# Performance work log

Measured on AMD Instinct MI355X. Metric: run time of the kernel, lower is better.

The kernel has to match this reference:

```python
import jax, jax.numpy as jnp
import numpy as np

D_MODEL, D_K, D_V, H = 1024, 64, 64, 16
B, NQ, NK = 4, 1024, 1024


def setup_inputs() -> dict:
    key = jax.random.key(0)
    ks = jax.random.split(key, 16)
    xav = lambda k, shape: jax.random.uniform(k, shape, jnp.float32, -1.0, 1.0) * np.sqrt(6.0 / (shape[0] + shape[1])).astype(np.float32)
    return {
        "queries": jax.random.normal(ks[0], (B, NQ, D_MODEL), jnp.float32),
        "keys": jax.random.normal(ks[1], (B, NK, D_MODEL), jnp.float32),
        "values": jax.random.normal(ks[2], (B, NK, D_MODEL), jnp.float32),
        "attention_weights": jax.random.uniform(ks[3], (B, H, NQ, NK), jnp.float32),
        "attention_mask": jax.random.randint(ks[4], (B, H, NQ, NK), 0, 2, jnp.int32),
        "Wq": xav(ks[5], (H * D_K, D_MODEL)), "bq": jnp.zeros((H * D_K,), jnp.float32),
        "Wk": xav(ks[6], (H * D_K, D_MODEL)), "bk": jnp.zeros((H * D_K,), jnp.float32),
        "Wv": xav(ks[7], (H * D_V, D_MODEL)), "bv": jnp.zeros((H * D_V,), jnp.float32),
        "Wo": xav(ks[8], (D_MODEL, H * D_V)), "bo": jnp.zeros((D_MODEL,), jnp.float32),
    }


def reference(queries, keys, values, attention_weights, attention_mask,
              Wq, bq, Wk, bk, Wv, bv, Wo, bo):
    b, nq, _ = queries.shape
    nk = keys.shape[1]
    # projections, split heads: (b, h, n, d)
    q = (queries @ Wq.T + bq).reshape(b, nq, H, D_K).transpose(0, 2, 1, 3)
    k = (keys @ Wk.T + bk).reshape(b, nk, H, D_K).transpose(0, 2, 1, 3)
    v = (values @ Wv.T + bv).reshape(b, nk, H, D_V).transpose(0, 2, 1, 3)
    scale = jnp.asarray(1.0 / np.sqrt(D_K), q.dtype)
    att = jnp.einsum('bhqd,bhkd->bhqk', q, k) * scale
    att_map = att  # returned pre-bias/mask scores, as in the torch code (att.clone())
    # way='mul', use_knn=False path
    att = att * attention_weights
    att = jnp.where(attention_mask == 0, -jnp.inf, att)
    att = jax.nn.softmax(att, axis=-1)
    out = jnp.einsum('bhqk,bhkd->bqhd', att, v).reshape(b, nq, H * D_V)
    out = out @ Wo.T + bo
    return out, att_map
```

## Files before the change

kernel.cpp:

```cpp
#include <hip/hip_runtime.h>
#include <stdint.h>
#include <math.h>

#define B_ 4
#define H_ 16
#define DM_ 1024
#define NQ_ 1024
#define NK_ 1024

typedef __attribute__((ext_vector_type(4))) float f32x4;
typedef __attribute__((ext_vector_type(4))) int   s32x4;
typedef __attribute__((ext_vector_type(4))) short s16x4;
typedef __attribute__((ext_vector_type(8))) short s16x8;

#define MFMA(a, b, c) __builtin_amdgcn_mfma_f32_16x16x32_bf16(a, b, c, 0, 0, 0)

static __device__ __forceinline__ short f2bf(float f) {
  union { float f; uint32_t u; } v; v.f = f;
  uint32_t r = (v.u + 0x7FFFu + ((v.u >> 16) & 1u)) >> 16;
  return (short)(uint16_t)r;
}

static __device__ __forceinline__ float bf2f(short s) {
  union { uint32_t u; float f; } v;
  v.u = ((uint32_t)(uint16_t)s) << 16;
  return v.f;
}

static __device__ __forceinline__ void gload_lds16(const void* g, void* s) {
  __builtin_amdgcn_global_load_lds(
      (const __attribute__((address_space(1))) uint32_t*)g,
      (__attribute__((address_space(3))) uint32_t*)s, 16, 0, 0);
}

__global__ void k_cvt(const float* __restrict__ src, short* __restrict__ dst, int n) {
  int i = (blockIdx.x * 256 + threadIdx.x) * 4;
  if (i + 3 < n) {
    f32x4 v = *(const f32x4*)(src + i);
    s16x4 o;
    o.x = f2bf(v.x); o.y = f2bf(v.y); o.z = f2bf(v.z); o.w = f2bf(v.w);
    *(s16x4*)(dst + i) = o;
  }
}

__global__ __launch_bounds__(256, 2) void k_gemm(
    const short* __restrict__ A, const short* __restrict__ Bw,
    const float* __restrict__ bias, void* __restrict__ outp, int mode) {
  __shared__ short As[128 * 64];
  __shared__ short Bs[128 * 64];
  const int tid = threadIdx.x;
  const int w = tid >> 6, l = tid & 63;
  const int wm = w >> 1, wn = w & 1;
  const int lr = l & 15, lg = l >> 4;
  const int m0 = blockIdx.x * 128, n0 = blockIdx.y * 128;

  f32x4 acc[4][4] = {};

  for (int kt = 0; kt < 16; ++kt) {
    __syncthreads();
#pragma unroll
    for (int q = 0; q < 4; ++q) {
      const int slot = (w * 4 + q) * 64 + l;
      const int row = slot >> 3;
      const int chunk = (slot & 7) ^ (row & 7);
      const size_t goff = (size_t)row * 1024 + (size_t)kt * 64 + chunk * 8;
      gload_lds16(A + (size_t)m0 * 1024 + goff, (char*)As + (w * 4 + q) * 1024);
      gload_lds16(Bw + (size_t)n0 * 1024 + goff, (char*)Bs + (w * 4 + q) * 1024);
    }
    asm volatile("s_waitcnt vmcnt(0)");
    __syncthreads();
#pragma unroll
    for (int ks = 0; ks < 2; ++ks) {
      s16x8 af[4], bfr[4];
#pragma unroll
      for (int mi = 0; mi < 4; ++mi) {
        const int row = wm * 64 + mi * 16 + lr;
        const int chunk = (ks * 4 + lg) ^ (row & 7);
        af[mi] = *(const s16x8*)(As + row * 64 + chunk * 8);
      }
#pragma unroll
      for (int ni = 0; ni < 4; ++ni) {
        const int row = wn * 64 + ni * 16 + lr;
        const int chunk = (ks * 4 + lg) ^ (row & 7);
        bfr[ni] = *(const s16x8*)(Bs + row * 64 + chunk * 8);
      }
#pragma unroll
      for (int mi = 0; mi < 4; ++mi)
#pragma unroll
        for (int ni = 0; ni < 4; ++ni)
          acc[mi][ni] = MFMA(af[mi], bfr[ni], acc[mi][ni]);
    }
  }

#pragma unroll
  for (int mi = 0; mi < 4; ++mi) {
#pragma unroll
    for (int ni = 0; ni < 4; ++ni) {
      const int gm0 = m0 + wm * 64 + mi * 16 + lg * 4;
      const int gc = n0 + wn * 64 + ni * 16 + lr;
      const float bv = bias[gc];
      if (mode == 2) {
        float* o = (float*)outp;
#pragma unroll
        for (int r = 0; r < 4; ++r)
          o[(size_t)(gm0 + r) * 1024 + gc] = acc[mi][ni][r] + bv;
      } else if (mode == 0) {
        short* o = (short*)outp;
        const int h = gc >> 6, d = gc & 63;
#pragma unroll
        for (int r = 0; r < 4; ++r) {
          const int gm = gm0 + r;
          const int b = gm >> 10, np = gm & 1023;
          o[((size_t)(b * 16 + h) * 1024 + np) * 64 + d] = f2bf(acc[mi][ni][r] + bv);
        }
      } else {
        short* o = (short*)outp;
        const int h = gc >> 6, d = gc & 63;
        const int b = gm0 >> 10, np0 = gm0 & 1023;
        s16x4 pk;
        pk.x = f2bf(acc[mi][ni][0] + bv);
        pk.y = f2bf(acc[mi][ni][1] + bv);
        pk.z = f2bf(acc[mi][ni][2] + bv);
        pk.w = f2bf(acc[mi][ni][3] + bv);
        *(s16x4*)(o + ((size_t)(b * 16 + h) * 64 + d) * 1024 + np0) = pk;
      }
    }
  }
}

__global__ __launch_bounds__(256, 3) void k_attn(
    const short* __restrict__ qws, const short* __restrict__ kws,
    const short* __restrict__ vtws,
    const float* __restrict__ attw, const int* __restrict__ attm,
    float* __restrict__ att_map, short* __restrict__ aout) {
  __shared__ f32x4 s_lds[4 * 256];
  __shared__ short p_lds[4 * 16 * 64];
  __shared__ float st_lds[4 * 16];
  const int tid = threadIdx.x;
  const int w = tid >> 6, l = tid & 63;
  const int lr = l & 15, lg = l >> 4;
  const int bh = blockIdx.y;
  const int q0 = blockIdx.x * 64 + w * 16;
  f32x4* const sw = s_lds + w * 256;
  char* const pw = (char*)p_lds + w * 2048;
  float* const stw = st_lds + w * 16;

  const short* qb = qws + ((size_t)bh * NQ_ + q0 + lr) * 64 + lg * 8;
  const s16x8 qf0 = *(const s16x8*)(qb);
  const s16x8 qf1 = *(const s16x8*)(qb + 32);

  f32x4 o[4] = {};
  float m4[4], l4[4];
#pragma unroll
  for (int it = 0; it < 4; ++it) { m4[it] = -3.0e38f; l4[it] = 0.0f; }

  const size_t linBase = ((size_t)bh * NQ_ + q0 + lg) * (size_t)NK_ + lr * 4;

  const int rot = (blockIdx.x + bh) & 15;

  for (int t = 0; t < 16; ++t) {
    const int kt = (rot + t) & 15;
    f32x4 s[4];
    const short* kb0 = kws + ((size_t)bh * NK_ + kt * 64 + lr) * 64 + lg * 8;
#pragma unroll
    for (int fn = 0; fn < 4; ++fn) {
      const short* kb = kb0 + fn * 1024;
      f32x4 z = {};
      z = MFMA(*(const s16x8*)kb, qf0, z);
      z = MFMA(*(const s16x8*)(kb + 32), qf1, z);
      s[fn] = z;
    }
#pragma unroll
    for (int fn = 0; fn < 4; ++fn)
      sw[lr * 16 + ((fn * 4 + lg) ^ lr)] = s[fn];
    asm volatile("s_waitcnt lgkmcnt(0)" ::: "memory");
    __builtin_amdgcn_sched_barrier(0);
    f32x4 sv4[4], wv4[4];
    s32x4 mv4[4];
#pragma unroll
    for (int it = 0; it < 4; ++it) {
      const int q = it * 4 + lg;
      sv4[it] = sw[q * 16 + (lr ^ q)];
      const size_t ga = linBase + (size_t)(it * 4) * NK_ + kt * 64;
      wv4[it] = *(const f32x4*)(attw + ga);
      mv4[it] = *(const s32x4*)(attm + ga);
    }
#pragma unroll
    for (int it = 0; it < 4; ++it) {
      const int q = it * 4 + lg;
      f32x4 sv;
#pragma unroll
      for (int j = 0; j < 4; ++j) sv[j] = sv4[it][j] * 0.125f;
      const size_t ga = linBase + (size_t)(it * 4) * NK_ + kt * 64;
      *(f32x4*)(att_map + ga) = sv;
      float p[4];
#pragma unroll
      for (int j = 0; j < 4; ++j)
        p[j] = mv4[it][j] ? sv[j] * wv4[it][j] : -1.0e30f;
      float t2 = fmaxf(fmaxf(p[0], p[1]), fmaxf(p[2], p[3]));
      t2 = fmaxf(t2, __shfl_xor(t2, 1, 64));
      t2 = fmaxf(t2, __shfl_xor(t2, 2, 64));
      t2 = fmaxf(t2, __shfl_xor(t2, 4, 64));
      t2 = fmaxf(t2, __shfl_xor(t2, 8, 64));
      const float mn = fmaxf(m4[it], t2);
      const float corr = __expf(m4[it] - mn);
      m4[it] = mn;
      float rs = 0.0f;
#pragma unroll
      for (int j = 0; j < 4; ++j) { p[j] = __expf(p[j] - mn); rs += p[j]; }
      rs += __shfl_xor(rs, 1, 64);
      rs += __shfl_xor(rs, 2, 64);
      rs += __shfl_xor(rs, 4, 64);
      rs += __shfl_xor(rs, 8, 64);
      l4[it] = l4[it] * corr + rs;
      s16x4 pk;
      pk.x = f2bf(p[0]); pk.y = f2bf(p[1]); pk.z = f2bf(p[2]); pk.w = f2bf(p[3]);
      *(s16x4*)(pw + q * 128 + (((lr >> 1) ^ (q & 7)) << 4) + (lr & 1) * 8) = pk;
      if (lr == 0) stw[q] = corr;
    }
    asm volatile("s_waitcnt lgkmcnt(0)" ::: "memory");
    __builtin_amdgcn_sched_barrier(0);
#pragma unroll
    for (int r = 0; r < 4; ++r) {
      const float cr = stw[lg * 4 + r];
      o[0][r] *= cr; o[1][r] *= cr; o[2][r] *= cr; o[3][r] *= cr;
    }
    const short* vb0 = vtws + ((size_t)bh * 64 + lr) * (size_t)NK_ + (size_t)kt * 64 + lg * 8;
#pragma unroll
    for (int ks = 0; ks < 2; ++ks) {
      const int chunk = (ks * 4 + lg) ^ (lr & 7);
      const s16x8 pa = *(const s16x8*)(pw + lr * 128 + chunk * 16);
#pragma unroll
      for (int g = 0; g < 4; ++g) {
        const s16x8 vf = *(const s16x8*)(vb0 + (size_t)g * 16 * NK_ + ks * 32);
        o[g] = MFMA(pa, vf, o[g]);
      }
    }
  }

  if (lr == 0) {
#pragma unroll
    for (int it = 0; it < 4; ++it) stw[it * 4 + lg] = 1.0f / l4[it];
  }
  asm volatile("s_waitcnt lgkmcnt(0)" ::: "memory");
  __builtin_amdgcn_sched_barrier(0);
  const int b = bh >> 4, h = bh & 15;
#pragma unroll
  for (int r = 0; r < 4; ++r) {
    const float inv = stw[lg * 4 + r];
    const size_t orow = ((size_t)b * NQ_ + q0 + lg * 4 + r) * 1024 + h * 64 + lr;
#pragma unroll
    for (int g = 0; g < 4; ++g)
      aout[orow + g * 16] = f2bf(o[g][r] * inv);
  }
}

extern "C" void kernel_launch(void* const* d_in, const int* in_sizes, int n_in,
                              void* d_out, int out_size, void* d_ws, size_t ws_size,
                              hipStream_t stream) {
  const float* queries = (const float*)d_in[0];
  const float* keys    = (const float*)d_in[1];
  const float* values  = (const float*)d_in[2];
  const float* attw    = (const float*)d_in[3];
  const int*   attm    = (const int*)d_in[4];
  const float* Wq = (const float*)d_in[5];
  const float* bq = (const float*)d_in[6];
  const float* Wk = (const float*)d_in[7];
  const float* bk = (const float*)d_in[8];
  const float* Wv = (const float*)d_in[9];
  const float* bv = (const float*)d_in[10];
  const float* Wo = (const float*)d_in[11];
  const float* bo = (const float*)d_in[12];

  float* out = (float*)d_out;
  float* att_map = out + (size_t)B_ * NQ_ * DM_;

  short* ws  = (short*)d_ws;
  short* WqB = ws;
  short* WkB = WqB + 1048576;
  short* WvB = WkB + 1048576;
  short* WoB = WvB + 1048576;
  short* Xq  = WoB + 1048576;
  short* Xk  = Xq + 4194304;
  short* Xv  = Xk + 4194304;
  short* qws = Xv + 4194304;
  short* kws = qws + 4194304;
  short* vtw = kws + 4194304;
  short* aout = vtw + 4194304;

  k_cvt<<<4096, 256, 0, stream>>>(queries, Xq, 4194304);
  k_cvt<<<4096, 256, 0, stream>>>(keys, Xk, 4194304);
  k_cvt<<<4096, 256, 0, stream>>>(values, Xv, 4194304);
  k_cvt<<<1024, 256, 0, stream>>>(Wq, WqB, 1048576);
  k_cvt<<<1024, 256, 0, stream>>>(Wk, WkB, 1048576);
  k_cvt<<<1024, 256, 0, stream>>>(Wv, WvB, 1048576);
  k_cvt<<<1024, 256, 0, stream>>>(Wo, WoB, 1048576);

  dim3 gg(32, 8);
  k_gemm<<<gg, 256, 0, stream>>>(Xq, WqB, bq, qws, 0);
  k_gemm<<<gg, 256, 0, stream>>>(Xk, WkB, bk, kws, 0);
  k_gemm<<<gg, 256, 0, stream>>>(Xv, WvB, bv, vtw, 1);

  dim3 ga(16, 64);
  k_attn<<<ga, 256, 0, stream>>>(qws, kws, vtw, attw, attm, att_map, aout);

  k_gemm<<<gg, 256, 0, stream>>>(aout, WoB, bo, out, 2);
}
```

Baseline: 346.3 us.

## Fuse fp32-to-bf16 activation conversion into projection GEMM loads, batch weight casts

The three standalone conversion kernels for queries, keys and values are removed. The Q/K/V projection GEMMs now read fp32 activations directly, convert them to bf16 in registers and store them into the swizzled shared-memory tile. The four weight conversions are merged into one launch with a 2D grid. This saves the bf16 activation round trip through global memory and several launches. In exchange the A-tile loads become synchronous register loads instead of direct global-to-LDS copies, and each 128x128 GEMM tile reads twice as many bytes. Every column block also re-converts the same A rows.

```diff
diff --git a/kernel.cpp b/kernel.cpp
--- a/kernel.cpp
+++ b/kernel.cpp
@@ -33,18 +33,26 @@
       (__attribute__((address_space(3))) uint32_t*)s, 16, 0, 0);
 }
 
-__global__ void k_cvt(const float* __restrict__ src, short* __restrict__ dst, int n) {
-  int i = (blockIdx.x * 256 + threadIdx.x) * 4;
-  if (i + 3 < n) {
-    f32x4 v = *(const f32x4*)(src + i);
-    s16x4 o;
-    o.x = f2bf(v.x); o.y = f2bf(v.y); o.z = f2bf(v.z); o.w = f2bf(v.w);
-    *(s16x4*)(dst + i) = o;
-  }
+__global__ void k_cvt4(const float* __restrict__ a, const float* __restrict__ b,
+                       const float* __restrict__ c, const float* __restrict__ d,
+                       short* __restrict__ o0, short* __restrict__ o1,
+                       short* __restrict__ o2, short* __restrict__ o3) {
+  const int i = (blockIdx.x * 256 + threadIdx.x) * 4;
+  const float* src; short* dst;
+  switch (blockIdx.y) {
+    case 0: src = a; dst = o0; break;
+    case 1: src = b; dst = o1; break;
+    case 2: src = c; dst = o2; break;
+    default: src = d; dst = o3; break;
+  }
+  f32x4 v = *(const f32x4*)(src + i);
+  s16x4 o;
+  o.x = f2bf(v.x); o.y = f2bf(v.y); o.z = f2bf(v.z); o.w = f2bf(v.w);
+  *(s16x4*)(dst + i) = o;
 }
 
 __global__ __launch_bounds__(256, 2) void k_gemm(
-    const short* __restrict__ A, const short* __restrict__ Bw,
+    const void* __restrict__ Asrc, const short* __restrict__ Bw,
     const float* __restrict__ bias, void* __restrict__ outp, int mode) {
   __shared__ short As[128 * 64];
   __shared__ short Bs[128 * 64];
@@ -58,13 +66,34 @@
 
   for (int kt = 0; kt < 16; ++kt) {
     __syncthreads();
+    if (mode < 2) {
+      const float* Af = (const float*)Asrc;
+#pragma unroll
+      for (int p = 0; p < 8; ++p) {
+        const int e = p * 1024 + tid * 4;
+        const int row = e >> 6, col = e & 63;
+        const f32x4 v = *(const f32x4*)(Af + (size_t)(m0 + row) * 1024 + kt * 64 + col);
+        s16x4 pk;
+        pk.x = f2bf(v.x); pk.y = f2bf(v.y); pk.z = f2bf(v.z); pk.w = f2bf(v.w);
+        *(s16x4*)((char*)As + row * 128 + (((col >> 3) ^ (row & 7)) << 4) + (col & 4) * 2) = pk;
+      }
+    } else {
+      const short* A = (const short*)Asrc;
+#pragma unroll
+      for (int q = 0; q < 4; ++q) {
+        const int slot = (w * 4 + q) * 64 + l;
+        const int row = slot >> 3;
+        const int chunk = (slot & 7) ^ (row & 7);
+        const size_t goff = (size_t)row * 1024 + (size_t)kt * 64 + chunk * 8;
+        gload_lds16(A + (size_t)m0 * 1024 + goff, (char*)As + (w * 4 + q) * 1024);
+      }
+    }
 #pragma unroll
     for (int q = 0; q < 4; ++q) {
       const int slot = (w * 4 + q) * 64 + l;
       const int row = slot >> 3;
       const int chunk = (slot & 7) ^ (row & 7);
       const size_t goff = (size_t)row * 1024 + (size_t)kt * 64 + chunk * 8;
-      gload_lds16(A + (size_t)m0 * 1024 + goff, (char*)As + (w * 4 + q) * 1024);
       gload_lds16(Bw + (size_t)n0 * 1024 + goff, (char*)Bs + (w * 4 + q) * 1024);
     }
     asm volatile("s_waitcnt vmcnt(0)");
@@ -280,26 +309,17 @@
   short* WkB = WqB + 1048576;
   short* WvB = WkB + 1048576;
   short* WoB = WvB + 1048576;
-  short* Xq  = WoB + 1048576;
-  short* Xk  = Xq + 4194304;
-  short* Xv  = Xk + 4194304;
-  short* qws = Xv + 4194304;
+  short* qws = WoB + 1048576;
   short* kws = qws + 4194304;
   short* vtw = kws + 4194304;
   short* aout = vtw + 4194304;
 
-  k_cvt<<<4096, 256, 0, stream>>>(queries, Xq, 4194304);
-  k_cvt<<<4096, 256, 0, stream>>>(keys, Xk, 4194304);
-  k_cvt<<<4096, 256, 0, stream>>>(values, Xv, 4194304);
-  k_cvt<<<1024, 256, 0, stream>>>(Wq, WqB, 1048576);
-  k_cvt<<<1024, 256, 0, stream>>>(Wk, WkB, 1048576);
-  k_cvt<<<1024, 256, 0, stream>>>(Wv, WvB, 1048576);
-  k_cvt<<<1024, 256, 0, stream>>>(Wo, WoB, 1048576);
+  k_cvt4<<<dim3(1024, 4), 256, 0, stream>>>(Wq, Wk, Wv, Wo, WqB, WkB, WvB, WoB);
 
   dim3 gg(32, 8);
-  k_gemm<<<gg, 256, 0, stream>>>(Xq, WqB, bq, qws, 0);
-  k_gemm<<<gg, 256, 0, stream>>>(Xk, WkB, bk, kws, 0);
-  k_gemm<<<gg, 256, 0, stream>>>(Xv, WvB, bv, vtw, 1);
+  k_gemm<<<gg, 256, 0, stream>>>(queries, WqB, bq, qws, 0);
+  k_gemm<<<gg, 256, 0, stream>>>(keys,    WkB, bk, kws, 0);
+  k_gemm<<<gg, 256, 0, stream>>>(values,  WvB, bv, vtw, 1);
 
   dim3 ga(16, 64);
   k_attn<<<ga, 256, 0, stream>>>(qws, kws, vtw, attw, attm, att_map, aout);
```

Result: slower. 494.9 us (+42.9%).
